# Kernel tuning notes

Hardware: AMD Instinct MI355X
Metric: run time of the kernel (lower is better)

## Reference

```python
import jax, jax.numpy as jnp
import numpy as np

D_MODEL = 2048
N_HEADS = 16
N_KV_HEADS = 4
HEAD_DIM = D_MODEL // N_HEADS  # 128
ROPE_THETA = 1000000.0


def _quant_rowwise(x):
    """Symmetric int8 rowwise quantization over the last dim (simulated in f32)."""
    s = jnp.max(jnp.abs(x), axis=-1, keepdims=True) / 127.0
    s = jnp.maximum(s, 1e-8)
    q = jnp.clip(jnp.round(x / s), -127.0, 127.0)
    return q, s


def _rope_tables(seq_len, head_dim, theta, dtype):
    inv_freq = 1.0 / (theta ** (jnp.arange(0, head_dim, 2, dtype=jnp.float32) / head_dim))
    pos = jnp.arange(seq_len, dtype=jnp.float32)
    freqs = pos[:, None] * inv_freq[None, :]            # (T, hd/2)
    emb = jnp.concatenate([freqs, freqs], axis=-1)      # (T, hd)
    return jnp.cos(emb).astype(dtype), jnp.sin(emb).astype(dtype)


def _rotate_half(x):
    h = x.shape[-1] // 2
    return jnp.concatenate([-x[..., h:], x[..., :h]], axis=-1)


def setup_inputs() -> dict:
    key = jax.random.key(0)
    k0, k1, k2, k3, k4 = jax.random.split(key, 5)
    x = jax.random.normal(k0, (1, 2048, D_MODEL), dtype=jnp.float32)
    sc = D_MODEL ** -0.5
    wq = jax.random.normal(k1, (N_HEADS * HEAD_DIM, D_MODEL), dtype=jnp.float32) * sc
    wk = jax.random.normal(k2, (N_KV_HEADS * HEAD_DIM, D_MODEL), dtype=jnp.float32) * sc
    wv = jax.random.normal(k3, (N_KV_HEADS * HEAD_DIM, D_MODEL), dtype=jnp.float32) * sc
    wo = jax.random.normal(k4, (D_MODEL, N_HEADS * HEAD_DIM), dtype=jnp.float32) * sc
    return {"x": x, "wq": wq, "wk": wk, "wv": wv, "wo": wo}


def _int8_linear(qx, x_scale, w):
    # Per-output-channel int8 weight quant, int8 matmul, rowwise dequant.
    qw, w_scale = _quant_rowwise(w)                      # (O,D), (O,1)
    y = jnp.einsum('btd,od->bto', qx, qw)
    return y * x_scale * w_scale[:, 0][None, None, :]


def reference(x, wq, wk, wv, wo):
    B, T, D = x.shape
    H, Hkv, hd = N_HEADS, N_KV_HEADS, HEAD_DIM
    scale = hd ** -0.5

    # Shared int8-quantized input for QKV projections
    qx, x_scale = _quant_rowwise(x)                      # (B,T,D), (B,T,1)
    q = _int8_linear(qx, x_scale, wq).reshape(B, T, H, hd).transpose(0, 2, 1, 3)
    k = _int8_linear(qx, x_scale, wk).reshape(B, T, Hkv, hd).transpose(0, 2, 1, 3)
    v = _int8_linear(qx, x_scale, wv).reshape(B, T, Hkv, hd).transpose(0, 2, 1, 3)

    # RoPE
    cos, sin = _rope_tables(T, hd, ROPE_THETA, x.dtype)  # (T, hd)
    q = q * cos + _rotate_half(q) * sin
    k = k * cos + _rotate_half(k) * sin

    # GQA: repeat kv heads
    rep = H // Hkv
    k = jnp.repeat(k, rep, axis=1)
    v = jnp.repeat(v, rep, axis=1)

    # int8 attention core: rowwise quantize q,k,v, int8 score matmul, dequant
    qq, qs = _quant_rowwise(q)
    kq, ks = _quant_rowwise(k)
    vq, vs = _quant_rowwise(v)
    scores = jnp.einsum('bhqd,bhkd->bhqk', qq, kq) * qs * jnp.swapaxes(ks, -1, -2) * scale
    causal = jnp.tril(jnp.ones((T, T), dtype=bool))
    scores = jnp.where(causal[None, None], scores, jnp.finfo(scores.dtype).min)
    attn = jax.nn.softmax(scores, axis=-1)
    out = jnp.einsum('bhqk,bhkd->bhqd', attn, vq * vs)   # dequant v inside matmul

    out = out.transpose(0, 2, 1, 3).reshape(B, T, H * hd)
    return out @ wo.T
```

## Files before the change

kernel.cpp:

```cpp
#include <hip/hip_runtime.h>
#include <cstdint>
#include <math.h>

#define TT 2048
#define DD 2048
#define NH 16
#define NKV 4
#define HD 128
#define SCALE_F 0.08838834764831845f
#define LOG2E 1.4426950408889634f

#if __has_builtin(__builtin_amdgcn_exp2f)
#define EXP2(x) __builtin_amdgcn_exp2f(x)
#else
#define EXP2(x) exp2f(x)
#endif

typedef int   i32x4 __attribute__((ext_vector_type(4)));
typedef float f32x4 __attribute__((ext_vector_type(4)));
typedef short s16x8 __attribute__((ext_vector_type(8)));

__device__ __forceinline__ i32x4 mfma_i8(i32x4 a, i32x4 b, i32x4 c) {
  return __builtin_amdgcn_mfma_i32_16x16x64_i8(a, b, c, 0, 0, 0);
}
__device__ __forceinline__ f32x4 mfma_bf16(s16x8 a, s16x8 b, f32x4 c) {
  return __builtin_amdgcn_mfma_f32_16x16x32_bf16(a, b, c, 0, 0, 0);
}
__device__ __forceinline__ uint32_t fbits(float f) {
  union { float f; uint32_t u; } x; x.f = f; return x.u;
}
__device__ __forceinline__ float bf16_to_f(ushort h) {
  union { uint32_t u; float f; } x; x.u = ((uint32_t)h) << 16; return x.f;
}

__global__ __launch_bounds__(256)
void quant_rows_kernel(const float* __restrict__ x, const float* __restrict__ wq,
                       const float* __restrict__ wk, const float* __restrict__ wv,
                       int8_t* __restrict__ qx, float* __restrict__ xs,
                       int8_t* __restrict__ qwq, float* __restrict__ wqs,
                       int8_t* __restrict__ qwk, float* __restrict__ wks,
                       int8_t* __restrict__ qwv, float* __restrict__ wvs,
                       float2* __restrict__ ropet) {
  int r = blockIdx.x;
  int tid = threadIdx.x;
  if (r >= 5120) {
    int idx = (r - 5120) * 256 + tid;
    int t = idx >> 6, d = idx & 63;
    float inv = 1.0f / powf(1000000.0f, (float)d * (1.0f/64.0f));
    float sn, cs;
    sincosf((float)t * inv, &sn, &cs);
    ropet[idx] = make_float2(cs, sn);
    return;
  }
  const float* src; int8_t* dst; float* sc; int row;
  if (r < 2048)      { src = x;  dst = qx;  sc = xs;  row = r; }
  else if (r < 4096) { src = wq; dst = qwq; sc = wqs; row = r - 2048; }
  else if (r < 4608) { src = wk; dst = qwk; sc = wks; row = r - 4096; }
  else               { src = wv; dst = qwv; sc = wvs; row = r - 4608; }
  src += (size_t)row * DD; dst += (size_t)row * DD;
  float4 v0 = ((const float4*)src)[2*tid];
  float4 v1 = ((const float4*)src)[2*tid+1];
  float m = fmaxf(fmaxf(fmaxf(fabsf(v0.x), fabsf(v0.y)), fmaxf(fabsf(v0.z), fabsf(v0.w))),
                  fmaxf(fmaxf(fabsf(v1.x), fabsf(v1.y)), fmaxf(fabsf(v1.z), fabsf(v1.w))));
  #pragma unroll
  for (int off = 1; off < 64; off <<= 1) m = fmaxf(m, __shfl_xor(m, off));
  __shared__ float wmax[4];
  if ((tid & 63) == 0) wmax[tid >> 6] = m;
  __syncthreads();
  m = fmaxf(fmaxf(wmax[0], wmax[1]), fmaxf(wmax[2], wmax[3]));
  float s = fmaxf(m / 127.0f, 1e-8f);
  if (tid == 0) sc[row] = s;
  float vv[8] = {v0.x, v0.y, v0.z, v0.w, v1.x, v1.y, v1.z, v1.w};
  uint32_t p0 = 0, p1 = 0;
  #pragma unroll
  for (int i = 0; i < 4; ++i) {
    int q = (int)fminf(fmaxf(rintf(vv[i] / s), -127.0f), 127.0f);
    p0 |= ((uint32_t)q & 0xffu) << (8*i);
  }
  #pragma unroll
  for (int i = 0; i < 4; ++i) {
    int q = (int)fminf(fmaxf(rintf(vv[4+i] / s), -127.0f), 127.0f);
    p1 |= ((uint32_t)q & 0xffu) << (8*i);
  }
  ((uint2*)dst)[tid] = make_uint2(p0, p1);
}

__global__ __launch_bounds__(256)
void proj_kernel(const int8_t* __restrict__ qx, const float* __restrict__ xs,
                 const int8_t* __restrict__ qwq, const float* __restrict__ wqs,
                 const int8_t* __restrict__ qwk, const float* __restrict__ wks,
                 const int8_t* __restrict__ qwv, const float* __restrict__ wvs,
                 const float2* __restrict__ ropet,
                 int8_t* __restrict__ qq, float* __restrict__ qsc_out,
                 int8_t* __restrict__ kq, float* __restrict__ ksc_out,
                 int8_t* __restrict__ vq, float* __restrict__ vsc_out) {
  int id  = blockIdx.x;
  int xcd = id & 7;
  int j   = id >> 3;
  int hg  = xcd >> 1;
  int th  = xcd & 1;
  int gh  = hg*6 + (j % 6);
  int tb  = th*16 + (j / 6);
  int t0  = tb * 64;

  const int8_t* wgt; const float* wsc; int8_t* outq; float* outs; bool doRope;
  if (gh < NH) {
    wgt = qwq + (size_t)gh*HD*DD; wsc = wqs + gh*HD;
    outq = qq + (size_t)gh*TT*HD; outs = qsc_out + (size_t)gh*TT; doRope = true;
  } else if (gh < NH + NKV) {
    int hh = gh - NH;
    wgt = qwk + (size_t)hh*HD*DD; wsc = wks + hh*HD;
    outq = kq + (size_t)hh*TT*HD; outs = ksc_out + (size_t)hh*TT; doRope = true;
  } else {
    int hh = gh - NH - NKV;
    wgt = qwv + (size_t)hh*HD*DD; wsc = wvs + hh*HD;
    outq = vq + (size_t)hh*TT*HD; outs = vsc_out + (size_t)hh*TT; doRope = false;
  }

  __shared__ int8_t As[64 * 144];
  __shared__ int8_t Bs[128 * 144];
  int tid = threadIdx.x;
  int w  = tid >> 6;
  int l  = tid & 63;
  int lg = l & 15;
  int lh = l >> 4;

  i32x4 acc[8];
  #pragma unroll
  for (int tj = 0; tj < 8; ++tj) acc[tj] = (i32x4){0,0,0,0};

  i32x4 prefA[2], prefB[4];

#define PROJ_ISSUE(KT)                                                          \
  {                                                                             \
    int kk0 = (KT) * 128;                                                       \
    _Pragma("unroll")                                                           \
    for (int i = 0; i < 2; ++i) {                                               \
      int idx = tid + i*256, r = idx >> 3, c = idx & 7;                         \
      prefA[i] = *(const i32x4*)&qx[(size_t)(t0 + r)*DD + kk0 + c*16];          \
    }                                                                           \
    _Pragma("unroll")                                                           \
    for (int i = 0; i < 4; ++i) {                                               \
      int idx = tid + i*256, r = idx >> 3, c = idx & 7;                         \
      prefB[i] = *(const i32x4*)&wgt[(size_t)r*DD + kk0 + c*16];                \
    }                                                                           \
  }

  PROJ_ISSUE(0);

  for (int kt = 0; kt < DD/128; ++kt) {
    __syncthreads();
    #pragma unroll
    for (int i = 0; i < 2; ++i) {
      int idx = tid + i*256, r = idx >> 3, c = idx & 7;
      *(i32x4*)&As[r*144 + c*16] = prefA[i];
    }
    #pragma unroll
    for (int i = 0; i < 4; ++i) {
      int idx = tid + i*256, r = idx >> 3, c = idx & 7;
      *(i32x4*)&Bs[r*144 + c*16] = prefB[i];
    }
    __syncthreads();
    if (kt + 1 < DD/128) PROJ_ISSUE(kt + 1);

    #pragma unroll
    for (int s = 0; s < 2; ++s) {
      i32x4 a0 = *(const i32x4*)&As[(w*16 + lg)*144 + s*64 + lh*16];
      #pragma unroll
      for (int tj = 0; tj < 8; ++tj) {
        i32x4 b = *(const i32x4*)&Bs[(tj*16 + lg)*144 + s*64 + lh*16];
        acc[tj] = mfma_i8(a0, b, acc[tj]);
      }
    }
  }
#undef PROJ_ISSUE

  float y[8][4];
  #pragma unroll
  for (int rr = 0; rr < 4; ++rr) {
    int tl = w*16 + lh*4 + rr;
    float xsi = xs[t0 + tl];
    #pragma unroll
    for (int tj = 0; tj < 8; ++tj)
      y[tj][rr] = (float)acc[tj][rr] * xsi * wsc[tj*16 + lg];
  }

  if (doRope) {
    #pragma unroll
    for (int rr = 0; rr < 4; ++rr) {
      int trow = t0 + w*16 + lh*4 + rr;
      const float2* tr = &ropet[trow * 64];
      #pragma unroll
      for (int tj = 0; tj < 4; ++tj) {
        float2 cssn = tr[tj*16 + lg];
        float lo = y[tj][rr], hi = y[tj+4][rr];
        y[tj][rr]   = lo*cssn.x - hi*cssn.y;
        y[tj+4][rr] = hi*cssn.x + lo*cssn.y;
      }
    }
  }

  __syncthreads();
  #pragma unroll
  for (int rr = 0; rr < 4; ++rr) {
    int tl = w*16 + lh*4 + rr;
    float mx = fabsf(y[0][rr]);
    #pragma unroll
    for (int tj = 1; tj < 8; ++tj) mx = fmaxf(mx, fabsf(y[tj][rr]));
    mx = fmaxf(mx, __shfl_xor(mx, 1));
    mx = fmaxf(mx, __shfl_xor(mx, 2));
    mx = fmaxf(mx, __shfl_xor(mx, 4));
    mx = fmaxf(mx, __shfl_xor(mx, 8));
    float s = fmaxf(mx / 127.0f, 1e-8f);
    if (lg == 0) outs[t0 + tl] = s;
    #pragma unroll
    for (int tj = 0; tj < 8; ++tj) {
      int qv = (int)fminf(fmaxf(rintf(y[tj][rr] / s), -127.0f), 127.0f);
      As[tl*144 + tj*16 + lg] = (int8_t)qv;
    }
  }
  __syncthreads();
  #pragma unroll
  for (int i = 0; i < 2; ++i) {
    int idx = tid + i*256, r = idx >> 3, c = idx & 7;
    *(i32x4*)&outq[(size_t)(t0 + r)*HD + c*16] = *(const i32x4*)&As[r*144 + c*16];
  }
}

__global__ __launch_bounds__(512)
void attn_mfma_kernel(const int8_t* __restrict__ qq, const float* __restrict__ qsc_in,
                      const int8_t* __restrict__ kq, const float* __restrict__ ksc_in,
                      const int8_t* __restrict__ vq, const float* __restrict__ vsc_in,
                      float* __restrict__ ao,
                      float* __restrict__ opA, float* __restrict__ opB,
                      float* __restrict__ ml) {
  int id = blockIdx.x;
  int h   = id / 30;
  int loc = id % 30;
  int qb2, c;
  if (loc < 12)      { qb2 = 15 - loc/3;        c = loc % 3; }
  else if (loc < 24) { qb2 = 11 - (loc - 12)/2; c = (loc - 12) % 2; }
  else               { qb2 = 5 - (loc - 24);    c = 0; }
  int nkt = 2*qb2 + 2;
  int nc  = (qb2 <= 5) ? 1 : ((qb2 <= 11) ? 2 : 3);
  int ktb = (c * nkt) / nc;
  int kte = ((c + 1) * nkt) / nc;
  int hk  = h >> 2;
  int qb0 = qb2 * 128;

  __shared__ int8_t Ks[64 * 144];
  __shared__ ushort Vt[128 * 72];
  __shared__ float  Pf[8][16 * 68];

  int tid = threadIdx.x;
  int w  = tid >> 6;
  int l  = tid & 63;
  int lg = l & 15;
  int lh = l >> 4;

  const int8_t* qp = &qq[((size_t)h*TT + qb0 + 16*w + lg)*HD + lh*16];
  i32x4 qa0 = *(const i32x4*)qp;
  i32x4 qa1 = *(const i32x4*)(qp + 64);

  int myq = qb0 + 16*w + lg;
  float qsl = qsc_in[(size_t)h*TT + myq] * (SCALE_F * LOG2E);

  float mrun = -1e30f, lrun = 0.f;
  f32x4 acc_o[8];
  #pragma unroll
  for (int dt = 0; dt < 8; ++dt) acc_o[dt] = (f32x4){0.f, 0.f, 0.f, 0.f};

  int sr = tid >> 3, scc = tid & 7;
  int m2 = tid & 31, d0 = (tid >> 5) * 8;

  i32x4 kreg;
  int2  vreg0, vreg1;

#define ISSUE_LOADS(KT)                                                         \
  {                                                                             \
    int kk0 = (KT) * 64;                                                        \
    kreg = *(const i32x4*)&kq[((size_t)hk*TT + kk0 + sr)*HD + scc*16];          \
    const int8_t* vp = &vq[((size_t)hk*TT + kk0 + 2*m2)*HD + d0];               \
    vreg0 = *(const int2*)vp;                                                   \
    vreg1 = *(const int2*)(vp + HD);                                            \
  }

  ISSUE_LOADS(ktb);

  for (int kt = ktb; kt < kte; ++kt) {
    int k0 = kt * 64;
    __syncthreads();
    *(i32x4*)&Ks[sr*144 + scc*16] = kreg;
    #pragma unroll
    for (int jj = 0; jj < 4; ++jj) {
      int a0 = (vreg0.x << (24 - 8*jj)) >> 24;
      int b0 = (vreg1.x << (24 - 8*jj)) >> 24;
      *(uint32_t*)&Vt[(d0 + jj)*72 + 2*m2] =
          (fbits((float)a0) >> 16) | ((fbits((float)b0) >> 16) << 16);
      int a1 = (vreg0.y << (24 - 8*jj)) >> 24;
      int b1 = (vreg1.y << (24 - 8*jj)) >> 24;
      *(uint32_t*)&Vt[(d0 + 4 + jj)*72 + 2*m2] =
          (fbits((float)a1) >> 16) | ((fbits((float)b1) >> 16) << 16);
    }
    __syncthreads();
    if (kt + 1 < kte) ISSUE_LOADS(kt + 1);

    i32x4 sacc[4];
    #pragma unroll
    for (int t = 0; t < 4; ++t) sacc[t] = (i32x4){0, 0, 0, 0};
    __builtin_amdgcn_s_setprio(1);
    #pragma unroll
    for (int t = 0; t < 4; ++t) {
      const int8_t* kp = &Ks[(16*t + lg)*144 + lh*16];
      i32x4 b0 = *(const i32x4*)kp;
      i32x4 b1 = *(const i32x4*)(kp + 64);
      sacc[t] = mfma_i8(b0, qa0, sacc[t]);
      sacc[t] = mfma_i8(b1, qa1, sacc[t]);
    }
    __builtin_amdgcn_s_setprio(0);

    f32x4 ksv4[4], vsv4[4];
    #pragma unroll
    for (int t = 0; t < 4; ++t) {
      ksv4[t] = *(const f32x4*)&ksc_in[(size_t)hk*TT + k0 + 16*t + 4*lh];
      vsv4[t] = *(const f32x4*)&vsc_in[(size_t)hk*TT + k0 + 16*t + 4*lh];
    }

    bool maskTile = (kt >= nkt - 2);
    float sf[4][4];
    #pragma unroll
    for (int t = 0; t < 4; ++t)
      #pragma unroll
      for (int rr = 0; rr < 4; ++rr) {
        float v = (float)sacc[t][rr] * qsl * ksv4[t][rr];
        if (maskTile) {
          int kkg = k0 + 16*t + 4*lh + rr;
          v = (kkg <= myq) ? v : -1e30f;
        }
        sf[t][rr] = v;
      }

    float rm = sf[0][0];
    #pragma unroll
    for (int t = 0; t < 4; ++t)
      #pragma unroll
      for (int rr = 0; rr < 4; ++rr) rm = fmaxf(rm, sf[t][rr]);
    rm = fmaxf(rm, __shfl_xor(rm, 16));
    rm = fmaxf(rm, __shfl_xor(rm, 32));

    bool defer = __all(rm <= mrun + 8.0f && mrun > -1e29f);
    float mnew, corr;
    if (defer) { mnew = mrun; corr = 1.0f; }
    else       { mnew = fmaxf(mrun, rm); corr = EXP2(mrun - mnew); mrun = mnew; }

    float p[4][4];
    float ps = 0.f;
    #pragma unroll
    for (int t = 0; t < 4; ++t)
      #pragma unroll
      for (int rr = 0; rr < 4; ++rr) { p[t][rr] = EXP2(sf[t][rr] - mnew); ps += p[t][rr]; }
    ps += __shfl_xor(ps, 16);
    ps += __shfl_xor(ps, 32);
    lrun = lrun * corr + ps;

    #pragma unroll
    for (int t = 0; t < 4; ++t) {
      f32x4 pw;
      #pragma unroll
      for (int rr = 0; rr < 4; ++rr) pw[rr] = p[t][rr] * vsv4[t][rr];
      *(f32x4*)&Pf[w][lg*68 + 16*t + 4*lh] = pw;
    }

    if (!defer) {
      #pragma unroll
      for (int dt = 0; dt < 8; ++dt)
        #pragma unroll
        for (int rr = 0; rr < 4; ++rr) acc_o[dt][rr] *= corr;
    }

    s16x8 pahi[2], palo[2];
    #pragma unroll
    for (int kb = 0; kb < 2; ++kb) {
      const float* pr = &Pf[w][lg*68 + kb*32 + lh*8];
      f32x4 x0 = *(const f32x4*)pr;
      f32x4 x1 = *(const f32x4*)(pr + 4);
      float xv[8] = {x0.x, x0.y, x0.z, x0.w, x1.x, x1.y, x1.z, x1.w};
      float lv[8];
      #pragma unroll
      for (int jv = 0; jv < 8; ++jv) {
        uint32_t hb = fbits(xv[jv]) & 0xffff0000u;
        union { uint32_t u; float f; } hf; hf.u = hb;
        lv[jv] = xv[jv] - hf.f;
      }
      union { uint32_t u[4]; s16x8 v; } H, L;
      #pragma unroll
      for (int jj = 0; jj < 4; ++jj) {
        H.u[jj] = (fbits(xv[2*jj]) >> 16) | (fbits(xv[2*jj+1]) & 0xffff0000u);
        L.u[jj] = (fbits(lv[2*jj]) >> 16) | (fbits(lv[2*jj+1]) & 0xffff0000u);
      }
      pahi[kb] = H.v; palo[kb] = L.v;
    }

    __builtin_amdgcn_s_setprio(1);
    #pragma unroll
    for (int dt = 0; dt < 8; ++dt) {
      #pragma unroll
      for (int kb = 0; kb < 2; ++kb) {
        s16x8 vb = *(const s16x8*)&Vt[(16*dt + lg)*72 + kb*32 + lh*8];
        acc_o[dt] = mfma_bf16(vb, pahi[kb], acc_o[dt]);
        acc_o[dt] = mfma_bf16(vb, palo[kb], acc_o[dt]);
      }
    }
    __builtin_amdgcn_s_setprio(0);
  }
#undef ISSUE_LOADS

  if (nc == 1) {
    float invv = 1.0f / lrun;
    size_t base = (size_t)myq*DD + (size_t)h*HD;
    #pragma unroll
    for (int dt = 0; dt < 8; ++dt) {
      f32x4 v;
      #pragma unroll
      for (int rr = 0; rr < 4; ++rr) v[rr] = acc_o[dt][rr] * invv;
      *(f32x4*)&ao[base + 16*dt + 4*lh] = v;
    }
  } else {
    int base = (qb2 <= 11) ? (qb2 - 6)*2 : 12 + (qb2 - 12)*3;
    int slot = h*24 + base + c;
    float* op = (slot < 160) ? (opA + (size_t)slot * 16384)
                             : (opB + (size_t)(slot - 160) * 16384);
    op += (size_t)(16*w + lg) * 128;
    #pragma unroll
    for (int dt = 0; dt < 8; ++dt)
      *(f32x4*)&op[16*dt + 4*lh] = acc_o[dt];
    if (lh == 0) {
      ml[slot*256 + 16*w + lg]       = mrun;
      ml[slot*256 + 128 + 16*w + lg] = lrun;
    }
  }
}

__global__ __launch_bounds__(256)
void merge_kernel(const float* __restrict__ opA, const float* __restrict__ opB,
                  const float* __restrict__ ml,
                  float* __restrict__ ao) {
  int tile = blockIdx.x;
  int h = tile / 10;
  int qb2 = 6 + tile % 10;
  int nc = (qb2 <= 11) ? 2 : 3;
  int sbase = h*24 + ((qb2 <= 11) ? (qb2 - 6)*2 : 12 + (qb2 - 12)*3);

  int tid = threadIdx.x;
  int row = tid >> 1;
  int cseg = (tid & 1) * 64;

  float mv[3], lv[3];
  const float* pp[3];
  #pragma unroll
  for (int i = 0; i < 3; ++i) {
    int slot = sbase + ((i < nc) ? i : 0);
    const float* p = (slot < 160) ? (opA + (size_t)slot * 16384)
                                  : (opB + (size_t)(slot - 160) * 16384);
    pp[i] = p + (size_t)row * 128 + cseg;
    if (i < nc) {
      mv[i] = ml[slot*256 + row];
      lv[i] = ml[slot*256 + 128 + row];
    } else {
      mv[i] = -1e30f;
      lv[i] = 0.f;
    }
  }
  float M = fmaxf(fmaxf(mv[0], mv[1]), mv[2]);
  float wgt[3];
  float L = 0.f;
  #pragma unroll
  for (int i = 0; i < 3; ++i) { wgt[i] = EXP2(mv[i] - M); L += wgt[i]*lv[i]; }
  float inv = 1.0f / L;

  size_t ob = (size_t)(qb2*128 + row)*DD + (size_t)h*HD + cseg;
  #pragma unroll
  for (int c4 = 0; c4 < 16; ++c4) {
    f32x4 a0 = *(const f32x4*)&pp[0][c4*4];
    f32x4 a1 = *(const f32x4*)&pp[1][c4*4];
    f32x4 a2 = *(const f32x4*)&pp[2][c4*4];
    f32x4 v;
    #pragma unroll
    for (int e = 0; e < 4; ++e)
      v[e] = (wgt[0]*a0[e] + wgt[1]*a1[e] + wgt[2]*a2[e]) * inv;
    *(f32x4*)&ao[ob + c4*4] = v;
  }
}

__global__ __launch_bounds__(256)
void awquant_kernel(const float* __restrict__ ao, const float* __restrict__ wom,
                    int8_t* __restrict__ ahi, int8_t* __restrict__ alo,
                    int8_t* __restrict__ bhi, int8_t* __restrict__ blo,
                    float* __restrict__ sa, float* __restrict__ sb) {
  int r = blockIdx.x;
  int tid = threadIdx.x;
  const float* src; int8_t* dhi; int8_t* dlo; float* sc; int row;
  if (r < 2048) { src = ao;  dhi = ahi; dlo = alo; sc = sa; row = r; }
  else          { src = wom; dhi = bhi; dlo = blo; sc = sb; row = r - 2048; }
  src += (size_t)row * DD;
  float4 a = ((const float4*)src)[2*tid];
  float4 b = ((const float4*)src)[2*tid+1];
  float v[8] = {a.x, a.y, a.z, a.w, b.x, b.y, b.z, b.w};
  float m = fabsf(v[0]);
  #pragma unroll
  for (int j = 1; j < 8; ++j) m = fmaxf(m, fabsf(v[j]));
  #pragma unroll
  for (int off = 1; off < 64; off <<= 1) m = fmaxf(m, __shfl_xor(m, off));
  __shared__ float wmax[4];
  if ((tid & 63) == 0) wmax[tid >> 6] = m;
  __syncthreads();
  m = fmaxf(fmaxf(wmax[0], wmax[1]), fmaxf(wmax[2], wmax[3]));
  float s = fmaxf(m * (1.0f/16256.0f), 1e-30f);
  if (tid == 0) sc[row] = s;
  float inv = 1.0f / s;
  uint32_t h0 = 0, h1 = 0, l0 = 0, l1 = 0;
  #pragma unroll
  for (int j = 0; j < 8; ++j) {
    float q = v[j] * inv;
    int hi = (int)fminf(fmaxf(rintf(q * (1.0f/128.0f)), -127.0f), 127.0f);
    int lo = (int)fminf(fmaxf(rintf(q - 128.0f*(float)hi), -127.0f), 127.0f);
    if (j < 4) { h0 |= ((uint32_t)hi & 0xffu) << (8*j);     l0 |= ((uint32_t)lo & 0xffu) << (8*j); }
    else       { h1 |= ((uint32_t)hi & 0xffu) << (8*(j-4)); l1 |= ((uint32_t)lo & 0xffu) << (8*(j-4)); }
  }
  ((uint2*)&dhi[(size_t)row*DD])[tid] = make_uint2(h0, h1);
  ((uint2*)&dlo[(size_t)row*DD])[tid] = make_uint2(l0, l1);
}

__global__ __launch_bounds__(256)
void wo_gemm_kernel(const int8_t* __restrict__ ahi, const int8_t* __restrict__ alo,
                    const int8_t* __restrict__ bhi, const int8_t* __restrict__ blo,
                    const float* __restrict__ sa, const float* __restrict__ sb,
                    float* __restrict__ outp) {
  int id  = blockIdx.x;
  int xcd = id & 7;
  int j   = id >> 3;
  int tb  = xcd*4 + (j >> 4);
  int ob  = j & 15;
  int t0  = tb * 64;
  int o0  = ob * 128;

  __shared__ int8_t AH[64 * 72];
  __shared__ int8_t AL[64 * 72];
  __shared__ int8_t BH[128 * 72];
  __shared__ int8_t BL[128 * 72];
  int tid = threadIdx.x;
  int wv4 = tid >> 6;
  int wr = wv4 >> 1, wc = wv4 & 1;
  int l  = tid & 63;
  int lg = l & 15;
  int lh = l >> 4;

  i32x4 acc_h[2][4], acc_m[2][4];
  #pragma unroll
  for (int ti = 0; ti < 2; ++ti)
    #pragma unroll
    for (int tj = 0; tj < 4; ++tj) {
      acc_h[ti][tj] = (i32x4){0,0,0,0};
      acc_m[ti][tj] = (i32x4){0,0,0,0};
    }

  i32x4 pAH, pAL, pBH[2], pBL[2];
  int ar = tid >> 2, ac = tid & 3;

#define WO_ISSUE(KT)                                                            \
  {                                                                             \
    int k0 = (KT) * 64;                                                         \
    size_t ga = (size_t)(t0 + ar)*DD + k0 + ac*16;                              \
    pAH = *(const i32x4*)&ahi[ga];                                              \
    pAL = *(const i32x4*)&alo[ga];                                              \
    _Pragma("unroll")                                                           \
    for (int i = 0; i < 2; ++i) {                                               \
      int idx = tid + i*256, r = idx >> 2, c = idx & 3;                         \
      size_t gb = (size_t)(o0 + r)*DD + k0 + c*16;                              \
      pBH[i] = *(const i32x4*)&bhi[gb];                                         \
      pBL[i] = *(const i32x4*)&blo[gb];                                         \
    }                                                                           \
  }

  WO_ISSUE(0);

  for (int kt = 0; kt < DD/64; ++kt) {
    __syncthreads();
    *(i32x4*)&AH[ar*72 + ac*16] = pAH;
    *(i32x4*)&AL[ar*72 + ac*16] = pAL;
    #pragma unroll
    for (int i = 0; i < 2; ++i) {
      int idx = tid + i*256, r = idx >> 2, c = idx & 3;
      *(i32x4*)&BH[r*72 + c*16] = pBH[i];
      *(i32x4*)&BL[r*72 + c*16] = pBL[i];
    }
    __syncthreads();
    if (kt + 1 < DD/64) WO_ISSUE(kt + 1);

    i32x4 a_h[2], a_l[2];
    #pragma unroll
    for (int ti = 0; ti < 2; ++ti) {
      int ab = (wr*32 + ti*16 + lg)*72 + lh*16;
      a_h[ti] = *(const i32x4*)&AH[ab];
      a_l[ti] = *(const i32x4*)&AL[ab];
    }
    __builtin_amdgcn_s_setprio(1);
    #pragma unroll
    for (int tj = 0; tj < 4; ++tj) {
      int bb = (wc*64 + tj*16 + lg)*72 + lh*16;
      i32x4 b_h = *(const i32x4*)&BH[bb];
      i32x4 b_l = *(const i32x4*)&BL[bb];
      #pragma unroll
      for (int ti = 0; ti < 2; ++ti) {
        acc_h[ti][tj] = mfma_i8(a_h[ti], b_h, acc_h[ti][tj]);
        acc_m[ti][tj] = mfma_i8(a_h[ti], b_l, acc_m[ti][tj]);
        acc_m[ti][tj] = mfma_i8(a_l[ti], b_h, acc_m[ti][tj]);
      }
    }
    __builtin_amdgcn_s_setprio(0);
  }
#undef WO_ISSUE

  #pragma unroll
  for (int ti = 0; ti < 2; ++ti) {
    float sav[4];
    #pragma unroll
    for (int rr = 0; rr < 4; ++rr)
      sav[rr] = sa[t0 + wr*32 + ti*16 + lh*4 + rr];
    #pragma unroll
    for (int tj = 0; tj < 4; ++tj) {
      int o = o0 + wc*64 + tj*16 + lg;
      float sbo = sb[o];
      #pragma unroll
      for (int rr = 0; rr < 4; ++rr) {
        int t = t0 + wr*32 + ti*16 + lh*4 + rr;
        float v = sav[rr] * sbo *
                  (16384.0f * (float)acc_h[ti][tj][rr] + 128.0f * (float)acc_m[ti][tj][rr]);
        outp[(size_t)t*DD + o] = v;
      }
    }
  }
}

extern "C" void kernel_launch(void* const* d_in, const int* in_sizes, int n_in,
                              void* d_out, int out_size, void* d_ws, size_t ws_size,
                              hipStream_t stream) {
  (void)in_sizes; (void)n_in; (void)out_size; (void)ws_size;
  const float* x  = (const float*)d_in[0];
  const float* wq = (const float*)d_in[1];
  const float* wk = (const float*)d_in[2];
  const float* wv = (const float*)d_in[3];
  const float* wo = (const float*)d_in[4];
  float* out = (float*)d_out;

  char* ws = (char*)d_ws;
  const size_t MB = 1048576;
  int8_t* qx  = (int8_t*)(ws);
  int8_t* qwq = (int8_t*)(ws + 4*MB);
  int8_t* qwk = (int8_t*)(ws + 8*MB);
  int8_t* qwv = (int8_t*)(ws + 9*MB);
  int8_t* qqp = (int8_t*)(ws + 10*MB);
  int8_t* kqp = (int8_t*)(ws + 14*MB);
  int8_t* vqp = (int8_t*)(ws + 15*MB);
  float* xs  = (float*)(ws + 16*MB);
  float* wqs = xs + 2048;
  float* wks = wqs + 2048;
  float* wvs = wks + 512;
  float* qsc = wvs + 512;
  float* ksc = qsc + (size_t)NH*TT;
  float* vsc = ksc + (size_t)NKV*TT;
  float* ao = (float*)(ws + 16*MB + 262144);
  float2* ropet = (float2*)(ws + 16*MB + 262144);
  float* opA = (float*)(ws);
  float* opB = out;
  float* mlb = (float*)((char*)out + 15*MB + 524288);
  int8_t* ahi = (int8_t*)(ws);
  int8_t* alo = (int8_t*)(ws + 4*MB);
  int8_t* bhi = (int8_t*)(ws + 8*MB);
  int8_t* blo = (int8_t*)(ws + 12*MB);
  float* sa = (float*)(ws + 16*MB);
  float* sb = sa + 2048;

  quant_rows_kernel<<<5632, 256, 0, stream>>>(x, wq, wk, wv,
                                              qx, xs, qwq, wqs, qwk, wks, qwv, wvs,
                                              ropet);
  proj_kernel<<<768, 256, 0, stream>>>(
      qx, xs, qwq, wqs, qwk, wks, qwv, wvs, ropet,
      qqp, qsc, kqp, ksc, vqp, vsc);
  attn_mfma_kernel<<<480, 512, 0, stream>>>(
      qqp, qsc, kqp, ksc, vqp, vsc, ao, opA, opB, mlb);
  merge_kernel<<<160, 256, 0, stream>>>(opA, opB, mlb, ao);
  awquant_kernel<<<4096, 256, 0, stream>>>(ao, wo, ahi, alo, bhi, blo, sa, sb);
  wo_gemm_kernel<<<512, 256, 0, stream>>>(ahi, alo, bhi, blo, sa, sb, out);
}
```

Measured before the change: 151.1 us.

## Double attention key tile to 128 and build P operands via shuffles

Result: slower. 164.1 us (+8.6%).

```diff
diff --git a/kernel.cpp b/kernel.cpp
--- a/kernel.cpp
+++ b/kernel.cpp
@@ -241,16 +241,15 @@
   if (loc < 12)      { qb2 = 15 - loc/3;        c = loc % 3; }
   else if (loc < 24) { qb2 = 11 - (loc - 12)/2; c = (loc - 12) % 2; }
   else               { qb2 = 5 - (loc - 24);    c = 0; }
-  int nkt = 2*qb2 + 2;
+  int nkt2 = qb2 + 1;
   int nc  = (qb2 <= 5) ? 1 : ((qb2 <= 11) ? 2 : 3);
-  int ktb = (c * nkt) / nc;
-  int kte = ((c + 1) * nkt) / nc;
+  int ktb = (c * nkt2) / nc;
+  int kte = ((c + 1) * nkt2) / nc;
   int hk  = h >> 2;
   int qb0 = qb2 * 128;
 
-  __shared__ int8_t Ks[64 * 144];
-  __shared__ ushort Vt[128 * 72];
-  __shared__ float  Pf[8][16 * 68];
+  __shared__ int8_t Ks[128 * 144];
+  __shared__ ushort Vt[128 * 136];
 
   int tid = threadIdx.x;
   int w  = tid >> 6;
@@ -270,47 +269,52 @@
   #pragma unroll
   for (int dt = 0; dt < 8; ++dt) acc_o[dt] = (f32x4){0.f, 0.f, 0.f, 0.f};
 
-  int sr = tid >> 3, scc = tid & 7;
-  int m2 = tid & 31, d0 = (tid >> 5) * 8;
-
-  i32x4 kreg;
-  int2  vreg0, vreg1;
+  int srow = tid >> 2, scol = (tid & 3) * 32;
+  int m2 = tid & 63, d0v = (tid >> 6) * 16;
+
+  i32x4 kregA, kregB;
+  int2  vr0a, vr0b, vr1a, vr1b;
 
 #define ISSUE_LOADS(KT)                                                         \
   {                                                                             \
-    int kk0 = (KT) * 64;                                                        \
-    kreg = *(const i32x4*)&kq[((size_t)hk*TT + kk0 + sr)*HD + scc*16];          \
-    const int8_t* vp = &vq[((size_t)hk*TT + kk0 + 2*m2)*HD + d0];               \
-    vreg0 = *(const int2*)vp;                                                   \
-    vreg1 = *(const int2*)(vp + HD);                                            \
+    int kk0 = (KT) * 128;                                                       \
+    const int8_t* kp0 = &kq[((size_t)hk*TT + kk0 + srow)*HD + scol];            \
+    kregA = *(const i32x4*)kp0;                                                 \
+    kregB = *(const i32x4*)(kp0 + 16);                                          \
+    const int8_t* vp = &vq[((size_t)hk*TT + kk0 + 2*m2)*HD + d0v];              \
+    vr0a = *(const int2*)vp;        vr0b = *(const int2*)(vp + 8);              \
+    vr1a = *(const int2*)(vp + HD); vr1b = *(const int2*)(vp + HD + 8);         \
   }
 
   ISSUE_LOADS(ktb);
 
   for (int kt = ktb; kt < kte; ++kt) {
-    int k0 = kt * 64;
+    int k0 = kt * 128;
     __syncthreads();
-    *(i32x4*)&Ks[sr*144 + scc*16] = kreg;
-    #pragma unroll
-    for (int jj = 0; jj < 4; ++jj) {
-      int a0 = (vreg0.x << (24 - 8*jj)) >> 24;
-      int b0 = (vreg1.x << (24 - 8*jj)) >> 24;
-      *(uint32_t*)&Vt[(d0 + jj)*72 + 2*m2] =
-          (fbits((float)a0) >> 16) | ((fbits((float)b0) >> 16) << 16);
-      int a1 = (vreg0.y << (24 - 8*jj)) >> 24;
-      int b1 = (vreg1.y << (24 - 8*jj)) >> 24;
-      *(uint32_t*)&Vt[(d0 + 4 + jj)*72 + 2*m2] =
-          (fbits((float)a1) >> 16) | ((fbits((float)b1) >> 16) << 16);
-    }
+    *(i32x4*)&Ks[srow*144 + scol]      = kregA;
+    *(i32x4*)&Ks[srow*144 + scol + 16] = kregB;
+#define VPACK(W0, W1, BASE)                                                     \
+    _Pragma("unroll")                                                           \
+    for (int jj = 0; jj < 4; ++jj) {                                            \
+      int a0 = ((W0) << (24 - 8*jj)) >> 24;                                     \
+      int b0 = ((W1) << (24 - 8*jj)) >> 24;                                     \
+      *(uint32_t*)&Vt[(d0v + (BASE) + jj)*136 + 2*m2] =                         \
+          (fbits((float)a0) >> 16) | ((fbits((float)b0) >> 16) << 16);          \
+    }
+    VPACK(vr0a.x, vr1a.x, 0)
+    VPACK(vr0a.y, vr1a.y, 4)
+    VPACK(vr0b.x, vr1b.x, 8)
+    VPACK(vr0b.y, vr1b.y, 12)
+#undef VPACK
     __syncthreads();
     if (kt + 1 < kte) ISSUE_LOADS(kt + 1);
 
-    i32x4 sacc[4];
-    #pragma unroll
-    for (int t = 0; t < 4; ++t) sacc[t] = (i32x4){0, 0, 0, 0};
+    i32x4 sacc[8];
+    #pragma unroll
+    for (int t = 0; t < 8; ++t) sacc[t] = (i32x4){0, 0, 0, 0};
     __builtin_amdgcn_s_setprio(1);
     #pragma unroll
-    for (int t = 0; t < 4; ++t) {
+    for (int t = 0; t < 8; ++t) {
       const int8_t* kp = &Ks[(16*t + lg)*144 + lh*16];
       i32x4 b0 = *(const i32x4*)kp;
       i32x4 b1 = *(const i32x4*)(kp + 64);
@@ -319,17 +323,17 @@
     }
     __builtin_amdgcn_s_setprio(0);
 
-    f32x4 ksv4[4], vsv4[4];
-    #pragma unroll
-    for (int t = 0; t < 4; ++t) {
+    f32x4 ksv4[8], vsv4[8];
+    #pragma unroll
+    for (int t = 0; t < 8; ++t) {
       ksv4[t] = *(const f32x4*)&ksc_in[(size_t)hk*TT + k0 + 16*t + 4*lh];
       vsv4[t] = *(const f32x4*)&vsc_in[(size_t)hk*TT + k0 + 16*t + 4*lh];
     }
 
-    bool maskTile = (kt >= nkt - 2);
-    float sf[4][4];
-    #pragma unroll
-    for (int t = 0; t < 4; ++t)
+    bool maskTile = (kt == nkt2 - 1);
+    float sf[8][4];
+    #pragma unroll
+    for (int t = 0; t < 8; ++t)
       #pragma unroll
       for (int rr = 0; rr < 4; ++rr) {
         float v = (float)sacc[t][rr] * qsl * ksv4[t][rr];
@@ -342,7 +346,7 @@
 
     float rm = sf[0][0];
     #pragma unroll
-    for (int t = 0; t < 4; ++t)
+    for (int t = 0; t < 8; ++t)
       #pragma unroll
       for (int rr = 0; rr < 4; ++rr) rm = fmaxf(rm, sf[t][rr]);
     rm = fmaxf(rm, __shfl_xor(rm, 16));
@@ -353,22 +357,27 @@
     if (defer) { mnew = mrun; corr = 1.0f; }
     else       { mnew = fmaxf(mrun, rm); corr = EXP2(mrun - mnew); mrun = mnew; }
 
-    float p[4][4];
+    float p[8][4];
     float ps = 0.f;
     #pragma unroll
-    for (int t = 0; t < 4; ++t)
+    for (int t = 0; t < 8; ++t)
       #pragma unroll
       for (int rr = 0; rr < 4; ++rr) { p[t][rr] = EXP2(sf[t][rr] - mnew); ps += p[t][rr]; }
     ps += __shfl_xor(ps, 16);
     ps += __shfl_xor(ps, 32);
     lrun = lrun * corr + ps;
 
-    #pragma unroll
-    for (int t = 0; t < 4; ++t) {
-      f32x4 pw;
-      #pragma unroll
-      for (int rr = 0; rr < 4; ++rr) pw[rr] = p[t][rr] * vsv4[t][rr];
-      *(f32x4*)&Pf[w][lg*68 + 16*t + 4*lh] = pw;
+    float pp0[4], pp1[4], pp2[4], pp3[4], pp4[4], pp5[4], pp6[4], pp7[4];
+    #pragma unroll
+    for (int rr = 0; rr < 4; ++rr) {
+      pp0[rr] = p[0][rr] * vsv4[0][rr];
+      pp1[rr] = p[1][rr] * vsv4[1][rr];
+      pp2[rr] = p[2][rr] * vsv4[2][rr];
+      pp3[rr] = p[3][rr] * vsv4[3][rr];
+      pp4[rr] = p[4][rr] * vsv4[4][rr];
+      pp5[rr] = p[5][rr] * vsv4[5][rr];
+      pp6[rr] = p[6][rr] * vsv4[6][rr];
+      pp7[rr] = p[7][rr] * vsv4[7][rr];
     }
 
     if (!defer) {
@@ -378,13 +387,26 @@
         for (int rr = 0; rr < 4; ++rr) acc_o[dt][rr] *= corr;
     }
 
-    s16x8 pahi[2], palo[2];
-    #pragma unroll
-    for (int kb = 0; kb < 2; ++kb) {
-      const float* pr = &Pf[w][lg*68 + kb*32 + lh*8];
-      f32x4 x0 = *(const f32x4*)pr;
-      f32x4 x1 = *(const f32x4*)(pr + 4);
-      float xv[8] = {x0.x, x0.y, x0.z, x0.w, x1.x, x1.y, x1.z, x1.w};
+    int srcA = lg + ((l & 16) << 1);
+    int srcB = srcA + 16;
+    bool hiT = (lh >= 2);
+    s16x8 pahi[4], palo[4];
+    #pragma unroll
+    for (int kb = 0; kb < 4; ++kb) {
+      float xv[8];
+      #pragma unroll
+      for (int rr = 0; rr < 4; ++rr) {
+        float se = (kb == 0) ? pp0[rr] : (kb == 1) ? pp2[rr]
+                 : (kb == 2) ? pp4[rr] : pp6[rr];
+        float so = (kb == 0) ? pp1[rr] : (kb == 1) ? pp3[rr]
+                 : (kb == 2) ? pp5[rr] : pp7[rr];
+        float loA = __shfl(se, srcA);
+        float hiA = __shfl(so, srcA);
+        float loB = __shfl(se, srcB);
+        float hiB = __shfl(so, srcB);
+        xv[rr]     = hiT ? hiA : loA;
+        xv[4 + rr] = hiT ? hiB : loB;
+      }
       float lv[8];
       #pragma unroll
       for (int jv = 0; jv < 8; ++jv) {
@@ -405,8 +427,8 @@
     #pragma unroll
     for (int dt = 0; dt < 8; ++dt) {
       #pragma unroll
-      for (int kb = 0; kb < 2; ++kb) {
-        s16x8 vb = *(const s16x8*)&Vt[(16*dt + lg)*72 + kb*32 + lh*8];
+      for (int kb = 0; kb < 4; ++kb) {
+        s16x8 vb = *(const s16x8*)&Vt[(16*dt + lg)*136 + kb*32 + lh*8];
         acc_o[dt] = mfma_bf16(vb, pahi[kb], acc_o[dt]);
         acc_o[dt] = mfma_bf16(vb, palo[kb], acc_o[dt]);
       }
```
